# Kernel tuning notes

Measured on AMD Instinct MI355X. Metric: run time of the kernel, lower is better.

Reference implementation:

```python
import jax, jax.numpy as jnp
import numpy as np

N_HEADS = 8
D_MODEL = 256
HEAD_DEPTH = D_MODEL // N_HEADS
B, S = 2, 4096


def setup_inputs() -> dict:
    key = jax.random.key(0)
    ks = jax.random.split(key, 8)
    scale = 1.0 / np.sqrt(D_MODEL)
    return {
        "q": jax.random.normal(ks[0], (B, S, D_MODEL), dtype=jnp.float32),
        "k": jax.random.normal(ks[1], (B, S, D_MODEL), dtype=jnp.float32),
        "v": jax.random.normal(ks[2], (B, S, D_MODEL), dtype=jnp.float32),
        "mask": jax.random.randint(ks[3], (B, S, S), 0, 2).astype(jnp.bool_),
        "wq": jax.random.normal(ks[4], (D_MODEL, D_MODEL), dtype=jnp.float32) * scale,
        "wk": jax.random.normal(ks[5], (D_MODEL, D_MODEL), dtype=jnp.float32) * scale,
        "wv": jax.random.normal(ks[6], (D_MODEL, D_MODEL), dtype=jnp.float32) * scale,
        "w_out": jax.random.normal(ks[7], (D_MODEL, D_MODEL), dtype=jnp.float32) * scale,
    }


def _split_heads(x):
    # [B, S, D] -> [B, H, S, Dh]
    b, s, _ = x.shape
    return x.reshape(b, s, N_HEADS, HEAD_DEPTH).transpose(0, 2, 1, 3)


def reference(q, k, v, mask, wq, wk, wv, w_out):
    Q = _split_heads(q @ wq)
    K = _split_heads(k @ wk)
    V = _split_heads(v @ wv)
    # [B, H, Sq, Sk]
    scores = jnp.einsum('bhqd,bhkd->bhqk', Q, K) / jnp.sqrt(
        jnp.asarray(HEAD_DEPTH, dtype=Q.dtype))
    # mask True -> -inf, broadcast over heads
    scores = jnp.where(mask[:, None, :, :], -jnp.inf, scores)
    probs = jax.nn.softmax(scores, axis=-1)
    attn = jnp.einsum('bhqk,bhkd->bhqd', probs, V)
    attn = attn.transpose(0, 2, 1, 3).reshape(q.shape[0], -1, D_MODEL)
    return attn @ w_out
```

## Files before the change

kernel.cpp:

```cpp
#include <hip/hip_runtime.h>
#include <stdint.h>

typedef __bf16 bf16;
typedef __bf16 bf16x8 __attribute__((ext_vector_type(8)));
typedef __bf16 bf16x4 __attribute__((ext_vector_type(4)));
typedef float  f32x4  __attribute__((ext_vector_type(4)));
typedef float  f32x16 __attribute__((ext_vector_type(16)));
typedef float  float4v __attribute__((ext_vector_type(4)));
typedef unsigned int uint;
typedef unsigned long long ull;

#define QSCALE 0.25505003984214403f


__global__ __launch_bounds__(256) void transpose_w(
    const float* __restrict__ w0, const float* __restrict__ w1,
    const float* __restrict__ w2, const float* __restrict__ w3,
    bf16* __restrict__ WT) {
  const int wsel = blockIdx.z;
  const float* W = wsel == 0 ? w0 : wsel == 1 ? w1 : wsel == 2 ? w2 : w3;
  const int k0 = blockIdx.x * 64, n0 = blockIdx.y * 64;
  __shared__ __align__(16) bf16 t[64][72];
  const int tid = threadIdx.x;
  {
    const int kk = (tid >> 4) << 2;
    const int nn = (tid & 15) << 2;
#pragma unroll
    for (int r = 0; r < 4; ++r) {
      float4v a = *(const float4v*)(W + (size_t)(k0 + kk + r) * 256 + n0 + nn);
#pragma unroll
      for (int j = 0; j < 4; ++j) t[nn + j][kk + r] = (bf16)a[j];
    }
  }
  __syncthreads();
  {
    const int ni = tid >> 2;
    const int c  = (tid & 3) * 16;
    bf16x8 o0 = *(const bf16x8*)(&t[ni][c]);
    bf16x8 o1 = *(const bf16x8*)(&t[ni][c + 8]);
    bf16* dst = WT + (size_t)wsel * 65536 + (size_t)(n0 + ni) * 256 + k0 + c;
    *(bf16x8*)dst = o0;
    *(bf16x8*)(dst + 8) = o1;
  }
}

__global__ __launch_bounds__(256) void proj_pack(
    const float* __restrict__ xq, const float* __restrict__ xk, const float* __restrict__ xv,
    const bf16* __restrict__ WT,
    bf16* __restrict__ Qp, bf16* __restrict__ Kp, bf16* __restrict__ Vp,
    const int* __restrict__ mask, uint* __restrict__ M2) {
  const int tid = threadIdx.x;
  if (blockIdx.x >= 768) {
    const int pid = blockIdx.x - 768;
    const int wid = pid * 4 + (tid >> 6);
    const int lane = tid & 63;
    const int row = wid >> 2, chunk = wid & 3;
    const int b = row >> 12, q = row & 4095;
    const size_t base = (size_t)row * 4096 + chunk * 1024 + lane;
    ull bl[16];
#pragma unroll
    for (int j = 0; j < 16; ++j) bl[j] = __ballot(mask[base + 64 * j] != 0);
    if (lane == 0) {
      uint* o = M2 + (size_t)b * 524288 + q;
#pragma unroll
      for (int j = 0; j < 16; ++j) {
        const int kdw = chunk * 32 + 2 * j;
        o[(size_t)kdw * 4096] = (uint)bl[j];
        o[(size_t)(kdw + 1) * 4096] = (uint)(bl[j] >> 32);
      }
    }
    return;
  }
  const int z = blockIdx.x >> 8;
  const int r8 = blockIdx.x & 255;
  const int m0 = (r8 >> 1) * 64, n0 = (r8 & 1) * 128;
  const float* X = z == 0 ? xq : (z == 1 ? xk : xv);
  const bf16* wt = WT + (size_t)z * 65536;
  const int wave = tid >> 6, lane = tid & 63;
  const int nl = lane & 15, quad = lane >> 4;
  const int arow = m0 + wave * 16 + nl;
  const float* xrow = X + (size_t)arow * 256;

  f32x4 zero4 = {0.f, 0.f, 0.f, 0.f};
  f32x4 acc[8];
#pragma unroll
  for (int i = 0; i < 8; ++i) acc[i] = zero4;

  for (int ks = 0; ks < 8; ++ks) {
    float4v a0 = *(const float4v*)(xrow + ks * 32 + quad * 8);
    float4v a1 = *(const float4v*)(xrow + ks * 32 + quad * 8 + 4);
    bf16x8 af;
#pragma unroll
    for (int i = 0; i < 4; ++i) { af[i] = (bf16)a0[i]; af[4 + i] = (bf16)a1[i]; }
#pragma unroll
    for (int nf = 0; nf < 8; ++nf) {
      bf16x8 bfr = *(const bf16x8*)(wt + (size_t)(n0 + nf * 16 + nl) * 256 + ks * 32 + quad * 8);
      acc[nf] = __builtin_amdgcn_mfma_f32_16x16x32_bf16(af, bfr, acc[nf], 0, 0, 0);
    }
  }

  const int Rbase = m0 + wave * 16 + quad * 4;
  if (z == 2) {
    const int b = Rbase >> 12, key = Rbase & 4095;
    const int key5 = key & 31;
    const int sub = ((key5 >> 4) << 1) | ((key5 >> 2) & 1);
    const int g = (key5 >> 3) & 1;
#pragma unroll
    for (int nf = 0; nf < 8; ++nf) {
      const int col = n0 + nf * 16 + nl;
      const int h = col >> 5, d = col & 31;
      bf16x4 o;
#pragma unroll
      for (int rr = 0; rr < 4; ++rr) o[rr] = (bf16)acc[nf][rr];
      const size_t off = (size_t)(b * 8 + h) * 131072 + (size_t)(key >> 5) * 1024 +
                         sub * 256 + d * 8 + g * 4;
      *(bf16x4*)(Vp + off) = o;
    }
  } else {
    const float scale = (z == 0) ? QSCALE : 1.0f;
    bf16* Out = z == 0 ? Qp : Kp;
#pragma unroll
    for (int nf = 0; nf < 8; ++nf) {
      const int col = n0 + nf * 16 + nl;
      const int h = col >> 5, d = col & 31;
      const int sub = d >> 3, j = d & 7;
#pragma unroll
      for (int rr = 0; rr < 4; ++rr) {
        const int R = Rbase + rr;
        const int b = R >> 12, sidx = R & 4095;
        const size_t off = (size_t)(b * 8 + h) * 131072 + (size_t)(sidx >> 5) * 1024 +
                           sub * 256 + (sidx & 31) * 8 + j;
        Out[off] = (bf16)(acc[nf][rr] * scale);
      }
    }
  }
}

__global__ __launch_bounds__(256) void attn_kernel(
    const bf16* __restrict__ Qp, const bf16* __restrict__ Kp,
    const bf16* __restrict__ Vp, const uint* __restrict__ M2,
    bf16* __restrict__ Og) {
  const int id = blockIdx.x;
  const int xcd = id & 7, slot = id >> 3;
  const int bh = xcd * 2 + (slot >> 6);
  const int q0 = (slot & 63) * 64;
  const int b = bh >> 3, h = bh & 7;
  const int tid = threadIdx.x, w = tid >> 6, lane = tid & 63;
  const int nl = lane & 31, half = lane >> 5;

  __shared__ float Ored[4][32][66];
  __shared__ float Lsum[64][8];

  const size_t bhbase = (size_t)bh * 131072;
  const int so0 = half * 256 + nl * 8;
  const int so1 = 512 + half * 256 + nl * 8;

  bf16x8 qf[2][2];
#pragma unroll
  for (int qt = 0; qt < 2; ++qt) {
    const bf16* qb = Qp + bhbase + (size_t)((q0 >> 5) + qt) * 1024;
    qf[qt][0] = *(const bf16x8*)(qb + so0);
    qf[qt][1] = *(const bf16x8*)(qb + so1);
  }

  const bf16* Kw = Kp + bhbase + (size_t)w * 1024;
  const bf16* Vw = Vp + bhbase + (size_t)w * 1024;
  const uint* Mw = M2 + (size_t)b * 524288 + (size_t)w * 4096 + q0 + nl;

  f32x16 z16;
#pragma unroll
  for (int i = 0; i < 16; ++i) z16[i] = 0.f;
  f32x16 acc0 = z16, acc1 = z16;
  float lsum0 = 0.f, lsum1 = 0.f;

  struct Frag { bf16x8 ka0, ka1, va0, va1; uint m0, m1; };
  auto LOADF = [&](int kt) -> Frag {
    Frag f;
    const bf16* kc = Kw + (size_t)kt * 4096;
    const bf16* vc = Vw + (size_t)kt * 4096;
    f.ka0 = *(const bf16x8*)(kc + so0);
    f.ka1 = *(const bf16x8*)(kc + so1);
    f.va0 = *(const bf16x8*)(vc + so0);
    f.va1 = *(const bf16x8*)(vc + so1);
    const uint* mp = Mw + (size_t)kt * 16384;
    f.m0 = mp[0];
    f.m1 = mp[32];
    return f;
  };

  auto STEP = [&](const Frag& f) {
    const int minv0 = (int)((~f.m0) >> (4 * half));
    const int minv1 = (int)((~f.m1) >> (4 * half));
    f32x16 st0 = __builtin_amdgcn_mfma_f32_32x32x16_bf16(f.ka0, qf[0][0], z16, 0, 0, 0);
    st0 = __builtin_amdgcn_mfma_f32_32x32x16_bf16(f.ka1, qf[0][1], st0, 0, 0, 0);
    f32x16 st1 = __builtin_amdgcn_mfma_f32_32x32x16_bf16(f.ka0, qf[1][0], z16, 0, 0, 0);
    st1 = __builtin_amdgcn_mfma_f32_32x32x16_bf16(f.ka1, qf[1][1], st1, 0, 0, 0);

    bf16 pe0[16], pe1[16];
#pragma unroll
    for (int g = 0; g < 4; ++g)
#pragma unroll
      for (int r = 0; r < 4; ++r) {
        const int i = g * 4 + r, off = r + 8 * g;
        float e0 = __builtin_amdgcn_exp2f(st0[i]);
        float e1 = __builtin_amdgcn_exp2f(st1[i]);
        const uint k0m = (uint)__builtin_amdgcn_sbfe(minv0, off, 1);
        const uint k1m = (uint)__builtin_amdgcn_sbfe(minv1, off, 1);
        e0 = __uint_as_float(__float_as_uint(e0) & k0m);
        e1 = __uint_as_float(__float_as_uint(e1) & k1m);
        lsum0 += e0; lsum1 += e1;
        pe0[i] = (bf16)e0; pe1[i] = (bf16)e1;
      }
    const bf16x8 pb00 = *(const bf16x8*)&pe0[0];
    const bf16x8 pb01 = *(const bf16x8*)&pe0[8];
    const bf16x8 pb10 = *(const bf16x8*)&pe1[0];
    const bf16x8 pb11 = *(const bf16x8*)&pe1[8];

    acc0 = __builtin_amdgcn_mfma_f32_32x32x16_bf16(f.va0, pb00, acc0, 0, 0, 0);
    acc0 = __builtin_amdgcn_mfma_f32_32x32x16_bf16(f.va1, pb01, acc0, 0, 0, 0);
    acc1 = __builtin_amdgcn_mfma_f32_32x32x16_bf16(f.va0, pb10, acc1, 0, 0, 0);
    acc1 = __builtin_amdgcn_mfma_f32_32x32x16_bf16(f.va1, pb11, acc1, 0, 0, 0);
  };

  Frag fa = LOADF(0), fb;
  for (int kt = 0; kt < 32; kt += 2) {
    fb = LOADF(kt + 1);
    STEP(fa);
    if (kt + 2 < 32) fa = LOADF(kt + 2);
    STEP(fb);
  }

#pragma unroll
  for (int g = 0; g < 4; ++g)
#pragma unroll
    for (int r = 0; r < 4; ++r) {
      const int d = r + 8 * g + 4 * half, i = g * 4 + r;
      Ored[w][d][nl] = acc0[i];
      Ored[w][d][32 + nl] = acc1[i];
    }
  Lsum[nl][w * 2 + half] = lsum0;
  Lsum[32 + nl][w * 2 + half] = lsum1;
  __syncthreads();
  if (tid < 64) {
    float s = 0.f;
#pragma unroll
    for (int j = 0; j < 8; ++j) s += Lsum[tid][j];
    Lsum[tid][0] = 1.0f / s;
  }
  __syncthreads();
  {
    const int q = tid >> 2, db = (tid & 3) * 8;
    const float rl = Lsum[q][0];
    bf16x8 o;
#pragma unroll
    for (int dj = 0; dj < 8; ++dj) {
      const float s = Ored[0][db + dj][q] + Ored[1][db + dj][q] +
                      Ored[2][db + dj][q] + Ored[3][db + dj][q];
      o[dj] = (bf16)(s * rl);
    }
    *(bf16x8*)(Og + ((size_t)(b * 4096 + q0 + q)) * 256 + h * 32 + db) = o;
  }
}

__global__ __launch_bounds__(256) void gemm_out(
    const bf16* __restrict__ A, const bf16* __restrict__ WTo, float* __restrict__ C) {
  const int m0 = blockIdx.x * 64, n0 = blockIdx.y * 128;
  const int tid = threadIdx.x, wave = tid >> 6, lane = tid & 63;
  const int nl = lane & 15, quad = lane >> 4;
  const int arow = m0 + wave * 16 + nl;

  f32x4 zero4 = {0.f, 0.f, 0.f, 0.f};
  f32x4 acc[8];
#pragma unroll
  for (int i = 0; i < 8; ++i) acc[i] = zero4;

  for (int ks = 0; ks < 8; ++ks) {
    bf16x8 af = *(const bf16x8*)(A + (size_t)arow * 256 + ks * 32 + quad * 8);
#pragma unroll
    for (int nf = 0; nf < 8; ++nf) {
      bf16x8 bfr = *(const bf16x8*)(WTo + (size_t)(n0 + nf * 16 + nl) * 256 + ks * 32 + quad * 8);
      acc[nf] = __builtin_amdgcn_mfma_f32_16x16x32_bf16(af, bfr, acc[nf], 0, 0, 0);
    }
  }
  const int Rbase = m0 + wave * 16 + quad * 4;
#pragma unroll
  for (int nf = 0; nf < 8; ++nf)
#pragma unroll
    for (int r = 0; r < 4; ++r)
      C[(size_t)(Rbase + r) * 256 + n0 + nf * 16 + nl] = acc[nf][r];
}

extern "C" void kernel_launch(void* const* d_in, const int* in_sizes, int n_in,
                              void* d_out, int out_size, void* d_ws, size_t ws_size,
                              hipStream_t stream) {
  const float* q  = (const float*)d_in[0];
  const float* k  = (const float*)d_in[1];
  const float* v  = (const float*)d_in[2];
  const int*  mask = (const int*)d_in[3];
  const float* wq = (const float*)d_in[4];
  const float* wk = (const float*)d_in[5];
  const float* wv = (const float*)d_in[6];
  const float* wo = (const float*)d_in[7];
  float* out = (float*)d_out;

  uint8_t* ws = (uint8_t*)d_ws;
  bf16* WT = (bf16*)ws;
  bf16* Qp = (bf16*)(ws + (512u << 10));
  bf16* Kp = Qp + 2097152;
  bf16* Vp = Kp + 2097152;
  uint* Mb = (uint*)((uint8_t*)(Vp + 2097152));
  bf16* Ao = (bf16*)((uint8_t*)Mb + (4u << 20));

  transpose_w<<<dim3(4, 4, 4), 256, 0, stream>>>(wq, wk, wv, wo, WT);
  proj_pack<<<dim3(768 + 8192), 256, 0, stream>>>(q, k, v, WT, Qp, Kp, Vp, mask, Mb);
  attn_kernel<<<dim3(1024), 256, 0, stream>>>(Qp, Kp, Vp, Mb, Ao);
  gemm_out<<<dim3(128, 2), 256, 0, stream>>>(Ao, WT + 3 * 65536, out);
}
```

Baseline: 329.7 us.

## Vectorize mask bit-packing and stage Q/K/V repacking through shared memory

The mask packing path now has each thread read int4 vectors and build 32-bit words itself, replacing per-element ballots. The words are transposed through shared memory so that M2 is written with coalesced 16-byte stores, and the mask grid shrinks from 8192 to 512 blocks. The Q/K/V projection epilogues stage results in LDS so the scattered 2-byte stores become 16-byte vector stores. In addition, attention converts probabilities to bf16 with a vector convert, and gemm_out uses 64-wide N tiles for twice as many blocks. The cost is extra shared memory, a barrier per block and more work per mask block.

```diff
diff --git a/kernel.cpp b/kernel.cpp
--- a/kernel.cpp
+++ b/kernel.cpp
@@ -5,8 +5,10 @@
 typedef __bf16 bf16x8 __attribute__((ext_vector_type(8)));
 typedef __bf16 bf16x4 __attribute__((ext_vector_type(4)));
 typedef float  f32x4  __attribute__((ext_vector_type(4)));
+typedef float  f32x8  __attribute__((ext_vector_type(8)));
 typedef float  f32x16 __attribute__((ext_vector_type(16)));
 typedef float  float4v __attribute__((ext_vector_type(4)));
+typedef int    int4v   __attribute__((ext_vector_type(4)));
 typedef unsigned int uint;
 typedef unsigned long long ull;
 
@@ -49,28 +51,43 @@
     const bf16* __restrict__ WT,
     bf16* __restrict__ Qp, bf16* __restrict__ Kp, bf16* __restrict__ Vp,
     const int* __restrict__ mask, uint* __restrict__ M2) {
+  __shared__ __align__(16) unsigned char smem[18432];
   const int tid = threadIdx.x;
+
   if (blockIdx.x >= 768) {
+    uint* trans = (uint*)smem;
     const int pid = blockIdx.x - 768;
-    const int wid = pid * 4 + (tid >> 6);
-    const int lane = tid & 63;
-    const int row = wid >> 2, chunk = wid & 3;
-    const int b = row >> 12, q = row & 4095;
-    const size_t base = (size_t)row * 4096 + chunk * 1024 + lane;
-    ull bl[16];
-#pragma unroll
-    for (int j = 0; j < 16; ++j) bl[j] = __ballot(mask[base + 64 * j] != 0);
-    if (lane == 0) {
-      uint* o = M2 + (size_t)b * 524288 + q;
-#pragma unroll
-      for (int j = 0; j < 16; ++j) {
-        const int kdw = chunk * 32 + 2 * j;
-        o[(size_t)kdw * 4096] = (uint)bl[j];
-        o[(size_t)(kdw + 1) * 4096] = (uint)(bl[j] >> 32);
+    const int bb = pid >> 8;
+    const int qt = (pid >> 2) & 63, kc = pid & 3;
+    const int q0 = qt * 64;
+    const int w = tid >> 6, l = tid & 63;
+    const int qrow = q0 + w * 16 + (l >> 2);
+    const size_t rowbase = ((size_t)(bb * 4096 + qrow)) * 4096 + kc * 1024;
+#pragma unroll
+    for (int p = 0; p < 8; ++p) {
+      const int kdw = p * 4 + (l & 3);
+      const int4v* mp = (const int4v*)(mask + rowbase + kdw * 32);
+      uint bits = 0;
+#pragma unroll
+      for (int j = 0; j < 8; ++j) {
+        int4v m = mp[j];
+#pragma unroll
+        for (int i = 0; i < 4; ++i) bits |= (m[i] != 0 ? 1u : 0u) << (j * 4 + i);
       }
+      trans[kdw * 72 + w * 16 + (l >> 2)] = bits;
+    }
+    __syncthreads();
+    {
+      const int r = tid >> 3, c = (tid & 7) * 4;
+      int4v a = *(const int4v*)(trans + r * 72 + c);
+      int4v d = *(const int4v*)(trans + r * 72 + c + 32);
+      uint* o = M2 + ((size_t)(bb * 128 + kc * 32 + r)) * 4096 + q0;
+      *(int4v*)(o + c) = a;
+      *(int4v*)(o + c + 32) = d;
     }
     return;
   }
+
   const int z = blockIdx.x >> 8;
   const int r8 = blockIdx.x & 255;
   const int m0 = (r8 >> 1) * 64, n0 = (r8 & 1) * 128;
@@ -99,39 +116,57 @@
     }
   }
 
-  const int Rbase = m0 + wave * 16 + quad * 4;
+  const int bq = m0 >> 12;
+  const int s0 = m0 & 4095;
+  const int posl = wave * 16 + quad * 4;
+
   if (z == 2) {
-    const int b = Rbase >> 12, key = Rbase & 4095;
-    const int key5 = key & 31;
-    const int sub = ((key5 >> 4) << 1) | ((key5 >> 2) & 1);
-    const int g = (key5 >> 3) & 1;
+    bf16* tv = (bf16*)smem;
 #pragma unroll
     for (int nf = 0; nf < 8; ++nf) {
-      const int col = n0 + nf * 16 + nl;
-      const int h = col >> 5, d = col & 31;
+      const int col = nf * 16 + nl;
       bf16x4 o;
 #pragma unroll
       for (int rr = 0; rr < 4; ++rr) o[rr] = (bf16)acc[nf][rr];
-      const size_t off = (size_t)(b * 8 + h) * 131072 + (size_t)(key >> 5) * 1024 +
-                         sub * 256 + d * 8 + g * 4;
-      *(bf16x4*)(Vp + off) = o;
+      *(bf16x4*)(tv + (size_t)col * 72 + posl) = o;
+    }
+    __syncthreads();
+    const int h2 = tid >> 6, ln = tid & 63;
+    const int d = ln & 31, shalf = ln >> 5;
+    const int h = (n0 >> 5) + h2;
+    bf16* vb = Vp + (size_t)(bq * 8 + h) * 131072 + (size_t)(s0 >> 5) * 1024 + d * 8;
+#pragma unroll
+    for (int it = 0; it < 4; ++it) {
+      const int blk = it >> 1, sub = (it & 1) * 2 + shalf;
+      const int K0 = (sub >> 1) * 16 + (sub & 1) * 4;
+      const bf16* src = tv + (size_t)(h2 * 32 + d) * 72 + blk * 32 + K0;
+      bf16x4 g0 = *(const bf16x4*)(src);
+      bf16x4 g1 = *(const bf16x4*)(src + 8);
+      bf16x8 o;
+#pragma unroll
+      for (int j = 0; j < 4; ++j) { o[j] = g0[j]; o[4 + j] = g1[j]; }
+      *(bf16x8*)(vb + (size_t)blk * 1024 + sub * 256) = o;
     }
   } else {
+    bf16* tq = (bf16*)smem;
     const float scale = (z == 0) ? QSCALE : 1.0f;
+#pragma unroll
+    for (int nf = 0; nf < 8; ++nf) {
+      const int col = nf * 16 + nl;
+#pragma unroll
+      for (int rr = 0; rr < 4; ++rr)
+        tq[(size_t)(posl + rr) * 136 + col] = (bf16)(acc[nf][rr] * scale);
+    }
+    __syncthreads();
     bf16* Out = z == 0 ? Qp : Kp;
-#pragma unroll
-    for (int nf = 0; nf < 8; ++nf) {
-      const int col = n0 + nf * 16 + nl;
-      const int h = col >> 5, d = col & 31;
-      const int sub = d >> 3, j = d & 7;
-#pragma unroll
-      for (int rr = 0; rr < 4; ++rr) {
-        const int R = Rbase + rr;
-        const int b = R >> 12, sidx = R & 4095;
-        const size_t off = (size_t)(b * 8 + h) * 131072 + (size_t)(sidx >> 5) * 1024 +
-                           sub * 256 + (sidx & 31) * 8 + j;
-        Out[off] = (bf16)(acc[nf][rr] * scale);
-      }
+    const int h2 = tid >> 6, ln = tid & 63;
+    const int h = (n0 >> 5) + h2;
+    const int s = s0 + ln;
+    bf16* ob = Out + (size_t)(bq * 8 + h) * 131072 + (size_t)(s >> 5) * 1024 + (s & 31) * 8;
+#pragma unroll
+    for (int sub = 0; sub < 4; ++sub) {
+      bf16x8 o = *(const bf16x8*)(tq + (size_t)ln * 136 + h2 * 32 + sub * 8);
+      *(bf16x8*)(ob + sub * 256) = o;
     }
   }
 }
@@ -196,7 +231,7 @@
     f32x16 st1 = __builtin_amdgcn_mfma_f32_32x32x16_bf16(f.ka0, qf[1][0], z16, 0, 0, 0);
     st1 = __builtin_amdgcn_mfma_f32_32x32x16_bf16(f.ka1, qf[1][1], st1, 0, 0, 0);
 
-    bf16 pe0[16], pe1[16];
+    f32x16 pf0, pf1;
 #pragma unroll
     for (int g = 0; g < 4; ++g)
 #pragma unroll
@@ -209,12 +244,16 @@
         e0 = __uint_as_float(__float_as_uint(e0) & k0m);
         e1 = __uint_as_float(__float_as_uint(e1) & k1m);
         lsum0 += e0; lsum1 += e1;
-        pe0[i] = (bf16)e0; pe1[i] = (bf16)e1;
+        pf0[i] = e0; pf1[i] = e1;
       }
-    const bf16x8 pb00 = *(const bf16x8*)&pe0[0];
-    const bf16x8 pb01 = *(const bf16x8*)&pe0[8];
-    const bf16x8 pb10 = *(const bf16x8*)&pe1[0];
-    const bf16x8 pb11 = *(const bf16x8*)&pe1[8];
+    const bf16x8 pb00 = __builtin_convertvector(
+        __builtin_shufflevector(pf0, pf0, 0, 1, 2, 3, 4, 5, 6, 7), bf16x8);
+    const bf16x8 pb01 = __builtin_convertvector(
+        __builtin_shufflevector(pf0, pf0, 8, 9, 10, 11, 12, 13, 14, 15), bf16x8);
+    const bf16x8 pb10 = __builtin_convertvector(
+        __builtin_shufflevector(pf1, pf1, 0, 1, 2, 3, 4, 5, 6, 7), bf16x8);
+    const bf16x8 pb11 = __builtin_convertvector(
+        __builtin_shufflevector(pf1, pf1, 8, 9, 10, 11, 12, 13, 14, 15), bf16x8);
 
     acc0 = __builtin_amdgcn_mfma_f32_32x32x16_bf16(f.va0, pb00, acc0, 0, 0, 0);
     acc0 = __builtin_amdgcn_mfma_f32_32x32x16_bf16(f.va1, pb01, acc0, 0, 0, 0);
@@ -264,27 +303,27 @@
 
 __global__ __launch_bounds__(256) void gemm_out(
     const bf16* __restrict__ A, const bf16* __restrict__ WTo, float* __restrict__ C) {
-  const int m0 = blockIdx.x * 64, n0 = blockIdx.y * 128;
+  const int m0 = blockIdx.x * 64, n0 = blockIdx.y * 64;
   const int tid = threadIdx.x, wave = tid >> 6, lane = tid & 63;
   const int nl = lane & 15, quad = lane >> 4;
   const int arow = m0 + wave * 16 + nl;
 
   f32x4 zero4 = {0.f, 0.f, 0.f, 0.f};
-  f32x4 acc[8];
-#pragma unroll
-  for (int i = 0; i < 8; ++i) acc[i] = zero4;
+  f32x4 acc[4];
+#pragma unroll
+  for (int i = 0; i < 4; ++i) acc[i] = zero4;
 
   for (int ks = 0; ks < 8; ++ks) {
     bf16x8 af = *(const bf16x8*)(A + (size_t)arow * 256 + ks * 32 + quad * 8);
 #pragma unroll
-    for (int nf = 0; nf < 8; ++nf) {
+    for (int nf = 0; nf < 4; ++nf) {
       bf16x8 bfr = *(const bf16x8*)(WTo + (size_t)(n0 + nf * 16 + nl) * 256 + ks * 32 + quad * 8);
       acc[nf] = __builtin_amdgcn_mfma_f32_16x16x32_bf16(af, bfr, acc[nf], 0, 0, 0);
     }
   }
   const int Rbase = m0 + wave * 16 + quad * 4;
 #pragma unroll
-  for (int nf = 0; nf < 8; ++nf)
+  for (int nf = 0; nf < 4; ++nf)
 #pragma unroll
     for (int r = 0; r < 4; ++r)
       C[(size_t)(Rbase + r) * 256 + n0 + nf * 16 + nl] = acc[nf][r];
@@ -312,7 +351,7 @@
   bf16* Ao = (bf16*)((uint8_t*)Mb + (4u << 20));
 
   transpose_w<<<dim3(4, 4, 4), 256, 0, stream>>>(wq, wk, wv, wo, WT);
-  proj_pack<<<dim3(768 + 8192), 256, 0, stream>>>(q, k, v, WT, Qp, Kp, Vp, mask, Mb);
+  proj_pack<<<dim3(768 + 512), 256, 0, stream>>>(q, k, v, WT, Qp, Kp, Vp, mask, Mb);
   attn_kernel<<<dim3(1024), 256, 0, stream>>>(Qp, Kp, Vp, Mb, Ao);
-  gemm_out<<<dim3(128, 2), 256, 0, stream>>>(Ao, WT + 3 * 65536, out);
-}
+  gemm_out<<<dim3(128, 4), 256, 0, stream>>>(Ao, WT + 3 * 65536, out);
+}
```

Measured after the change: 327.3 us. About the same (-0.7%).
